# Kernel optimization log

Hardware: AMD Instinct MI355X
Metric: run time of the kernel (lower is better)

The kernel has to match this reference:

```python
import jax, jax.numpy as jnp
import numpy as np
import math

BATCH, SEQLEN, HID, STATE = 8, 4096, 1024, 64


def setup_inputs() -> dict:
    key = jax.random.key(0)
    k_u, k_a, k_b, k_c = jax.random.split(key, 4)
    u = jax.random.normal(k_u, (BATCH, SEQLEN, HID), dtype=jnp.float32)
    A = jax.random.normal(k_a, (HID, STATE), dtype=jnp.float32)
    Bm = jax.random.normal(k_b, (HID, STATE), dtype=jnp.float32)
    C = jax.random.normal(k_c, (HID, STATE), dtype=jnp.float32)
    Dv = jnp.zeros((HID,), dtype=jnp.float32)
    # buffer: dt = exp(linspace(log 1e-3, log 1e-1, state_size))
    dt = jnp.exp(jnp.linspace(math.log(0.001), math.log(0.1), STATE)).astype(jnp.float32)
    return {"u": u, "A": A, "Bm": Bm, "C": C, "Dv": Dv, "dt": dt}


def reference(u, A, Bm, C, Dv, dt):
    # Diagonal LTI SSM (ZOH discretization):
    #   A_cont = -exp(A)                         (Dh, N)
    #   dA = exp(A_cont * dt)                    (Dh, N)
    #   dB = Bm * (1 - dA) / (-A_cont)           (Dh, N)
    # recurrence: x_t = x_{t-1} * dA + u_t * dB;  y_t = sum_n C * x_t + Dv * u_t
    Aexp = jnp.exp(A)                 # -A_cont, positive
    dA = jnp.exp(-Aexp * dt[None, :])
    dB = Bm * (1.0 - dA) / Aexp

    B_, L, Dh = u.shape
    N = dA.shape[1]

    def step(x, u_t):
        # x: (B, Dh, N), u_t: (B, Dh)
        x = x * dA + u_t[..., None] * dB
        y = jnp.einsum('bdn,dn->bd', x, C)
        return x, y

    x0 = jnp.zeros((B_, Dh, N), dtype=u.dtype)
    _, ys = jax.lax.scan(step, x0, jnp.swapaxes(u, 0, 1))  # ys: (L, B, Dh)
    out = jnp.swapaxes(ys, 0, 1) + u * Dv[None, None, :]
    return out
```

## Files before the change

kernel.cpp:

```cpp
#include <hip/hip_runtime.h>
#include <math.h>

#define BATCH  8
#define SEQLEN 4096
#define HID    1024
#define STATE  64
#define NC     16
#define TC     (SEQLEN / NC)
#define TT     32
#define NTILE  (TC / TT)
#define DBLK   64
#define NS     16
#define NP     8
#define RB     8

typedef float f32x2 __attribute__((ext_vector_type(2)));
typedef float f32x4 __attribute__((ext_vector_type(4)));
typedef short bf16x8 __attribute__((ext_vector_type(8)));
typedef unsigned int u32x4 __attribute__((ext_vector_type(4)));

#define WS_PA   0
#define WS_PW   (256 * 1024)
#define WS_PE   (512 * 1024)
#define WS_PL2  (768 * 1024)
#define WS_ZL   (1ull  * 1024 * 1024)
#define WS_ZT   (36ull * 1024 * 1024)
#define WS_W2F  (56ull * 1024 * 1024)
#define WS_KRF  (92ull * 1024 * 1024)
#define WS_NEED (148ull * 1024 * 1024)

__device__ __forceinline__ unsigned int f2bf(float x) {
    unsigned int u = __builtin_bit_cast(unsigned int, x);
    u = (u + 0x7FFFu + ((u >> 16) & 1u)) >> 16;
    return u & 0xFFFFu;
}

__device__ __forceinline__ void gload_lds16(const void* g, void* l) {
    __builtin_amdgcn_global_load_lds((const __attribute__((address_space(1))) void*)g,
                                     (__attribute__((address_space(3))) void*)l,
                                     16, 0, 0);
}

__device__ __forceinline__ float quad_reduce_add(float y) {
    int t = __builtin_amdgcn_mov_dpp(__builtin_bit_cast(int, y), 0xB1, 0xF, 0xF, true);
    y += __builtin_bit_cast(float, t);
    t = __builtin_amdgcn_mov_dpp(__builtin_bit_cast(int, y), 0x4E, 0xF, 0xF, true);
    y += __builtin_bit_cast(float, t);
    return y;
}

__global__ void k0_params(const float* __restrict__ A, const float* __restrict__ Bm,
                          const float* __restrict__ C, const float* __restrict__ dt,
                          float* __restrict__ pa, float* __restrict__ pw,
                          float* __restrict__ pE, float* __restrict__ pl2) {
    int i = blockIdx.x * 256 + threadIdx.x;
    if (i >= HID * STATE) return;
    int n = i & (STATE - 1);
    float aexp = expf(A[i]);
    float dtn  = dt[n];
    float a    = expf(-aexp * dtn);
    pa[i]  = a;
    pw[i]  = C[i] * (Bm[i] * (1.0f - a) / aexp);
    pE[i]  = expf(-aexp * dtn * (float)TC);
    pl2[i] = -aexp * dtn * 1.44269504088896340736f;
}

__global__ __launch_bounds__(256, 3) void k1_locals(const float* __restrict__ u,
                                                    const float* __restrict__ pa,
                                                    float* __restrict__ zl) {
    __shared__ float utile[2][TT * DBLK];
    int bid  = blockIdx.x;
    int dset = bid & 15;
    int b    = (bid >> 4) & 7;
    int c    = bid >> 7;
    int w    = threadIdx.x >> 6;
    int lane = threadIdx.x & 63;
    int dl   = lane >> 2, p = lane & 3;
    int d    = dset * DBLK + w * 16 + dl;

    f32x2 a2[NP], z2[NP];
    {
        const f32x2* pap = (const f32x2*)(pa + (size_t)d * STATE + p * NS);
        #pragma unroll
        for (int j = 0; j < NP; j++) a2[j] = pap[j];
    }
    #pragma unroll
    for (int j = 0; j < NP; j++) { z2[j].x = 0.f; z2[j].y = 0.f; }

    const char* ubase = (const char*)(u + ((size_t)b * SEQLEN + (size_t)c * TC) * HID
                                        + (size_t)dset * DBLK);

    #define ISSUE_TILE(t, buf)                                                        \
        {                                                                             \
            _Pragma("unroll")                                                         \
            for (int k = 0; k < 2; k++) {                                             \
                int off = w * 2048 + k * 1024 + lane * 16;                            \
                int row = off >> 8;                                                   \
                int col = off & 255;                                                  \
                const float* src = (const float*)(ubase + ((size_t)((t) * TT + row)) * (HID * 4) + col); \
                float* dst = &utile[buf][w * 512 + k * 256];                           \
                gload_lds16(src, dst);                                                \
            }                                                                         \
        }

    ISSUE_TILE(0, 0);
    __syncthreads();
    int cur = 0;
    for (int tile = 0; tile < NTILE; ++tile) {
        if (tile + 1 < NTILE) ISSUE_TILE(tile + 1, cur ^ 1);
        const float* ut = &utile[cur][w * 16 + dl];
        #pragma unroll
        for (int r = 0; r < TT; r++) {
            float uss = ut[r * DBLK];
            f32x2 us; us.x = uss; us.y = uss;
            #pragma unroll
            for (int j = 0; j < NP; j++)
                z2[j] = __builtin_elementwise_fma(a2[j], z2[j], us);
        }
        __syncthreads();
        cur ^= 1;
    }

    f32x2* zp = (f32x2*)(zl + (((size_t)c * BATCH + b) * HID + d) * STATE + p * NS);
    #pragma unroll
    for (int j = 0; j < NP; j++) zp[j] = z2[j];
}

__global__ void k2_scan(const float* __restrict__ pE, float* __restrict__ zl) {
    int i  = blockIdx.x * 256 + threadIdx.x;
    int dn = i & (HID * STATE - 1);
    float E = pE[dn];
    size_t stride = (size_t)BATCH * HID * STATE;
    float g = zl[i];
    for (int c = 1; c < NC - 1; c++) {
        float v = zl[i + c * stride];
        g = fmaf(E, g, v);
        zl[i + c * stride] = g;
    }
}

__global__ void k2_zt(const float* __restrict__ pE, const float* __restrict__ zl,
                      unsigned short* __restrict__ ZT) {
    int i = blockIdx.x * 256 + threadIdx.x;
    int n = i & 63;
    int d = (i >> 6) & 1023;
    int b = i >> 16;
    float E = pE[d * 64 + n];
    size_t stride = (size_t)BATCH * HID * STATE;
    unsigned short* zt = ZT + (size_t)d * 8192 + (size_t)b * 1024 + n;
    zt[0] = 0;
    float g = zl[i];
    zt[64] = (unsigned short)f2bf(g);
    for (int c = 2; c < 16; c++) {
        g = fmaf(E, g, zl[i + (size_t)(c - 1) * stride]);
        zt[(size_t)c * 64] = (unsigned short)f2bf(g);
    }
}

__global__ void k_krf(const float* __restrict__ pw, const float* __restrict__ pl2,
                      const float* __restrict__ Dv, unsigned short* __restrict__ KRF) {
    __shared__ float wv[64], e2[64], K[256];
    int d = blockIdx.x, t = threadIdx.x;
    if (t < 64) { wv[t] = pw[d * 64 + t]; e2[t] = pl2[d * 64 + t]; }
    __syncthreads();
    float s = 0.0f;
    for (int n = 0; n < 64; n++) s += wv[n] * exp2f((float)t * e2[n]);
    if (t == 0) s += Dv[d];
    K[t] = s;
    __syncthreads();
    for (int idx = t; idx < 8192; idx += 256) {
        int j  = idx & 7;
        int ll = (idx >> 3) & 63;
        int m  = idx >> 9;
        int x  = (ll & 15) - 8 * (ll >> 4) + 16 * m - j;
        unsigned short v = 0;
        if (x >= 0) v = (unsigned short)f2bf(K[x]);
        KRF[(size_t)d * 8192 + idx] = v;
    }
}

__global__ void k_w2f(const float* __restrict__ pw, const float* __restrict__ pl2,
                      unsigned short* __restrict__ W2F) {
    __shared__ float wv[64], e2[64];
    int d = blockIdx.x, t = threadIdx.x;
    if (t < 64) { wv[t] = pw[d * 64 + t]; e2[t] = pl2[d * 64 + t]; }
    __syncthreads();
    for (int idx = t; idx < 16384; idx += 256) {
        int j  = idx & 7;
        int ll = (idx >> 3) & 63;
        int ns = (idx >> 9) & 1;
        int tt = idx >> 10;
        int n  = ns * 32 + 8 * (ll >> 4) + j;
        int tg = tt * 16 + (ll & 15);
        float val = wv[n] * exp2f((float)(tg + 1) * e2[n]);
        W2F[(size_t)d * 16384 + idx] = (unsigned short)f2bf(val);
    }
}

__global__ __launch_bounds__(1024, 1) void k3_mfma(const float* __restrict__ u,
                                                   const unsigned short* __restrict__ KRF,
                                                   const unsigned short* __restrict__ W2F,
                                                   const unsigned short* __restrict__ ZT,
                                                   float* __restrict__ out) {
    __shared__ __align__(16) char smem[131072];
    int bid = blockIdx.x;
    int dg  = bid & 63;
    int bcg = bid >> 6;
    int tid = threadIdx.x;
    int w   = tid >> 6;
    int l   = tid & 63;
    int g   = l >> 4, r16 = l & 15;
    int d   = dg * 16 + w;

    {
        int dl = tid & 15;
        int v  = (tid >> 4) & 63;
        int bc = v & 15;
        int sq = v >> 4;
        int gbc = bcg * 16 + bc;
        int bs = gbc >> 4, cs = gbc & 15;
        const float* up = u + ((size_t)(bs * SEQLEN + cs * TC + sq * 64)) * HID
                            + dg * 16 + dl;
        unsigned int rowb = (unsigned int)(dl * 16 + bc) * 512;
        #pragma unroll
        for (int kk = 0; kk < 8; kk++) {
            float uv[8];
            #pragma unroll
            for (int j = 0; j < 8; j++) uv[j] = up[(size_t)(kk * 8 + j) * HID];
            unsigned int pk[4];
            #pragma unroll
            for (int q = 0; q < 4; q++)
                pk[q] = f2bf(uv[2 * q]) | (f2bf(uv[2 * q + 1]) << 16);
            int sc   = sq * 8 + kk;
            int slot = (sc + 4 * (bc & 7) + 5 * dl) & 31;
            *(u32x4*)(&smem[rowb + slot * 16]) = (u32x4){pk[0], pk[1], pk[2], pk[3]};
        }
    }
    __syncthreads();

    f32x4 acc[16];
    #pragma unroll
    for (int tt = 0; tt < 16; tt++) acc[tt] = (f32x4){0.f, 0.f, 0.f, 0.f};

    const unsigned short* krf = KRF + (size_t)d * 8192 + l * 8;
    unsigned int rowr = (unsigned int)(w * 16 + r16) * 512;
    int rot = (4 * (r16 & 7) + 5 * w) & 31;

    {
        bf16x8 Af[8];
        #pragma unroll
        for (int mm = 0; mm < 8; mm++)
            Af[mm] = *(const bf16x8*)(krf + (size_t)mm * 512);
        #pragma unroll
        for (int mm = 0; mm < 8; mm++) {
            #pragma unroll
            for (int sk = 0; sk < 8; sk++) {
                if (2 * sk + mm <= 15) {
                    int slot = ((sk * 4 + g) + rot) & 31;
                    bf16x8 B = *(const bf16x8*)(&smem[rowr + slot * 16]);
                    acc[2 * sk + mm] =
                        __builtin_amdgcn_mfma_f32_16x16x32_bf16(Af[mm], B, acc[2 * sk + mm], 0, 0, 0);
                }
            }
        }
    }
    __builtin_amdgcn_sched_barrier(0);
    {
        bf16x8 Af[8];
        #pragma unroll
        for (int mm = 0; mm < 8; mm++)
            Af[mm] = *(const bf16x8*)(krf + (size_t)(8 + mm) * 512);
        #pragma unroll
        for (int mm = 0; mm < 8; mm++) {
            #pragma unroll
            for (int sk = 0; sk < 4; sk++) {
                if (2 * sk + 8 + mm <= 15) {
                    int slot = ((sk * 4 + g) + rot) & 31;
                    bf16x8 B = *(const bf16x8*)(&smem[rowr + slot * 16]);
                    acc[2 * sk + 8 + mm] =
                        __builtin_amdgcn_mfma_f32_16x16x32_bf16(Af[mm], B, acc[2 * sk + 8 + mm], 0, 0, 0);
                }
            }
        }
    }
    __builtin_amdgcn_sched_barrier(0);

    {
        const unsigned short* ztd = ZT + (size_t)d * 8192 + (size_t)bcg * 1024;
        bf16x8 Bz0 = *(const bf16x8*)(ztd + (size_t)r16 * 64 + 0 * 32 + 8 * g);
        bf16x8 Bz1 = *(const bf16x8*)(ztd + (size_t)r16 * 64 + 1 * 32 + 8 * g);
        const unsigned short* w2f = W2F + (size_t)d * 16384 + l * 8;
        #pragma unroll
        for (int grp = 0; grp < 4; grp++) {
            bf16x8 Aw[8];
            #pragma unroll
            for (int q = 0; q < 8; q++) {
                int tt = grp * 4 + (q >> 1);
                int ns = q & 1;
                Aw[q] = *(const bf16x8*)(w2f + (size_t)(tt * 2 + ns) * 512);
            }
            #pragma unroll
            for (int q = 0; q < 8; q++) {
                int tt = grp * 4 + (q >> 1);
                acc[grp * 4 + (q >> 1)] =
                    __builtin_amdgcn_mfma_f32_16x16x32_bf16(Aw[q], (q & 1) ? Bz1 : Bz0,
                                                            acc[tt], 0, 0, 0);
            }
            __builtin_amdgcn_sched_barrier(0);
        }
    }

    float* eps = (float*)smem;
    int p = tid >> 2, sub = tid & 3;
    int t16r = p >> 4, bcr = p & 15;
    int gbcr = bcg * 16 + bcr;
    int bo = gbcr >> 4, co = gbcr & 15;
    float* pout = out + ((size_t)(bo * SEQLEN + co * TC + t16r)) * HID + dg * 16 + sub * 4;
    #pragma unroll
    for (int tt = 0; tt < 16; tt++) {
        __syncthreads();
        #pragma unroll
        for (int rr = 0; rr < 4; rr++)
            eps[((g * 4 + rr) * 16 + r16) * 21 + w] = acc[tt][rr];
        __syncthreads();
        f32x4 vv;
        #pragma unroll
        for (int j = 0; j < 4; j++) vv[j] = eps[p * 21 + sub * 4 + j];
        *(f32x4*)(pout + (size_t)(tt * 16) * HID) = vv;
    }
}

__global__ __launch_bounds__(256, 3) void k3_scalar(const float* __restrict__ u,
                                                    const float* __restrict__ Dv,
                                                    const float* __restrict__ pa,
                                                    const float* __restrict__ pw,
                                                    const float* __restrict__ zl,
                                                    float* __restrict__ out) {
    __shared__ float utile[2][TT * DBLK];
    int bid  = blockIdx.x;
    int dset = bid & 15;
    int b    = (bid >> 4) & 7;
    int c    = bid >> 7;
    int w    = threadIdx.x >> 6;
    int lane = threadIdx.x & 63;
    int dl   = lane >> 2, p = lane & 3;
    int d    = dset * DBLK + w * 16 + dl;

    f32x2 a2[NP], w2[NP], z2[NP];
    {
        const f32x2* pap = (const f32x2*)(pa + (size_t)d * STATE + p * NS);
        const f32x2* pwp = (const f32x2*)(pw + (size_t)d * STATE + p * NS);
        #pragma unroll
        for (int j = 0; j < NP; j++) { a2[j] = pap[j]; w2[j] = pwp[j]; }
    }
    if (c == 0) {
        #pragma unroll
        for (int j = 0; j < NP; j++) { z2[j].x = 0.f; z2[j].y = 0.f; }
    } else {
        size_t stride = (size_t)BATCH * HID * STATE;
        const f32x2* zp = (const f32x2*)(zl + (size_t)(c - 1) * stride +
                                         ((size_t)b * HID + d) * STATE + p * NS);
        #pragma unroll
        for (int j = 0; j < NP; j++) z2[j] = zp[j];
    }

    float dvd = Dv[d];
    const char* ubase = (const char*)(u + ((size_t)b * SEQLEN + (size_t)c * TC) * HID
                                        + (size_t)dset * DBLK);
    float* po = out + ((size_t)b * SEQLEN + (size_t)c * TC) * HID + d;

    ISSUE_TILE(0, 0);
    __syncthreads();
    int cur = 0;
    for (int tile = 0; tile < NTILE; ++tile) {
        if (tile + 1 < NTILE) ISSUE_TILE(tile + 1, cur ^ 1);
        const float* ut = &utile[cur][w * 16 + dl];
        float* po_t = po + (size_t)tile * TT * HID;
        #pragma unroll
        for (int r0 = 0; r0 < TT; r0 += RB) {
            float ylane[RB], usv[RB];
            #pragma unroll
            for (int i = 0; i < RB; i++) {
                float uss = ut[(r0 + i) * DBLK];
                usv[i] = uss;
                f32x2 us; us.x = uss; us.y = uss;
                #pragma unroll
                for (int j = 0; j < NP; j++)
                    z2[j] = __builtin_elementwise_fma(a2[j], z2[j], us);
                f32x2 acc0 = z2[0] * w2[0];
                f32x2 acc1 = z2[1] * w2[1];
                #pragma unroll
                for (int j = 2; j < NP; j += 2) {
                    acc0 = __builtin_elementwise_fma(z2[j + 0], w2[j + 0], acc0);
                    acc1 = __builtin_elementwise_fma(z2[j + 1], w2[j + 1], acc1);
                }
                acc0 += acc1;
                ylane[i] = acc0.x + acc0.y;
            }
            #pragma unroll
            for (int i = 0; i < RB; i++) ylane[i] = quad_reduce_add(ylane[i]);
            #pragma unroll
            for (int i = 0; i < RB; i++)
                po_t[(size_t)(r0 + i) * HID] = fmaf(dvd, usv[i], ylane[i]);
        }
        __syncthreads();
        cur ^= 1;
    }
}

extern "C" void kernel_launch(void* const* d_in, const int* in_sizes, int n_in,
                              void* d_out, int out_size, void* d_ws, size_t ws_size,
                              hipStream_t stream) {
    const float* u  = (const float*)d_in[0];
    const float* A  = (const float*)d_in[1];
    const float* Bm = (const float*)d_in[2];
    const float* C  = (const float*)d_in[3];
    const float* Dv = (const float*)d_in[4];
    const float* dt = (const float*)d_in[5];
    float* out = (float*)d_out;

    char* ws = (char*)d_ws;
    float* pa  = (float*)(ws + WS_PA);
    float* pw  = (float*)(ws + WS_PW);
    float* pE  = (float*)(ws + WS_PE);
    float* pl2 = (float*)(ws + WS_PL2);
    float* zl  = (float*)(ws + WS_ZL);
    unsigned short* ZT  = (unsigned short*)(ws + WS_ZT);
    unsigned short* W2F = (unsigned short*)(ws + WS_W2F);
    unsigned short* KRF = (unsigned short*)(ws + WS_KRF);

    bool mfma = (ws_size >= WS_NEED);

    k0_params<<<(HID * STATE) / 256, 256, 0, stream>>>(A, Bm, C, dt, pa, pw, pE, pl2);
    k1_locals<<<16 * 8 * (NC - 1), 256, 0, stream>>>(u, pa, zl);

    if (mfma) {
        k_krf<<<1024, 256, 0, stream>>>(pw, pl2, Dv, KRF);
        k_w2f<<<1024, 256, 0, stream>>>(pw, pl2, W2F);
        k2_zt<<<(BATCH * HID * STATE) / 256, 256, 0, stream>>>(pE, zl, ZT);
        k3_mfma<<<512, 1024, 0, stream>>>(u, KRF, W2F, ZT, out);
    } else {
        k2_scan<<<(BATCH * HID * STATE) / 256, 256, 0, stream>>>(pE, zl);
        k3_scalar<<<16 * 8 * NC, 256, 0, stream>>>(u, Dv, pa, pw, zl, out);
    }
}
```

Measured before the change: 180.2 us.

## Halve k3_mfma block to 8 hidden channels, vectorize u loads, remap block order

The MFMA output kernel now uses 512-thread blocks covering 8 hidden channels instead of 16, with 64KB shared memory, and launches twice as many blocks. This lets more blocks be resident per CU. The u tile is staged with float4 loads instead of scalar strided loads, and the LDS swizzle and epilogue padding are re-derived for the new shape. Block indices are permuted so neighbouring blocks touch interleaved channel groups, which may change L2 or channel locality. The risk is worse output coalescing, since each row now writes only 32 bytes per block, and more redundant loads of ZT and KRF.

New measurement: 235.1 us. +30.5%, slower.

```diff
diff --git a/kernel.cpp b/kernel.cpp
--- a/kernel.cpp
+++ b/kernel.cpp
@@ -197,43 +197,49 @@
     }
 }
 
-__global__ __launch_bounds__(1024, 1) void k3_mfma(const float* __restrict__ u,
-                                                   const unsigned short* __restrict__ KRF,
-                                                   const unsigned short* __restrict__ W2F,
-                                                   const unsigned short* __restrict__ ZT,
-                                                   float* __restrict__ out) {
-    __shared__ __align__(16) char smem[131072];
+__global__ __launch_bounds__(512, 4) void k3_mfma(const float* __restrict__ u,
+                                                  const unsigned short* __restrict__ KRF,
+                                                  const unsigned short* __restrict__ W2F,
+                                                  const unsigned short* __restrict__ ZT,
+                                                  float* __restrict__ out) {
+    __shared__ __align__(16) char smem[65536];
     int bid = blockIdx.x;
-    int dg  = bid & 63;
-    int bcg = bid >> 6;
+    int qx  = bid & 7;
+    int r   = bid >> 3;
+    int p   = r & 15;
+    int bcg = r >> 4;
+    int dg  = (((p & 7) * 8 + qx) << 1) | (p >> 3);
     int tid = threadIdx.x;
     int w   = tid >> 6;
     int l   = tid & 63;
     int g   = l >> 4, r16 = l & 15;
-    int d   = dg * 16 + w;
-
-    {
-        int dl = tid & 15;
-        int v  = (tid >> 4) & 63;
-        int bc = v & 15;
-        int sq = v >> 4;
+    int d   = dg * 8 + w;
+
+    {
+        int dq = tid & 1;
+        int bc = (tid >> 1) & 15;
+        int sg = tid >> 5;
         int gbc = bcg * 16 + bc;
         int bs = gbc >> 4, cs = gbc & 15;
-        const float* up = u + ((size_t)(bs * SEQLEN + cs * TC + sq * 64)) * HID
-                            + dg * 16 + dl;
-        unsigned int rowb = (unsigned int)(dl * 16 + bc) * 512;
-        #pragma unroll
-        for (int kk = 0; kk < 8; kk++) {
-            float uv[8];
-            #pragma unroll
-            for (int j = 0; j < 8; j++) uv[j] = up[(size_t)(kk * 8 + j) * HID];
-            unsigned int pk[4];
-            #pragma unroll
-            for (int q = 0; q < 4; q++)
-                pk[q] = f2bf(uv[2 * q]) | (f2bf(uv[2 * q + 1]) << 16);
-            int sc   = sq * 8 + kk;
-            int slot = (sc + 4 * (bc & 7) + 5 * dl) & 31;
-            *(u32x4*)(&smem[rowb + slot * 16]) = (u32x4){pk[0], pk[1], pk[2], pk[3]};
+        const f32x4* up = (const f32x4*)(u + ((size_t)(bs * SEQLEN + cs * TC + sg * 16)) * HID
+                                           + dg * 8 + dq * 4);
+        #pragma unroll
+        for (int half = 0; half < 2; half++) {
+            f32x4 v[8];
+            #pragma unroll
+            for (int j = 0; j < 8; j++) v[j] = up[(size_t)(half * 8 + j) * 256];
+            #pragma unroll
+            for (int dd = 0; dd < 4; dd++) {
+                unsigned int pk[4];
+                #pragma unroll
+                for (int q = 0; q < 4; q++)
+                    pk[q] = f2bf(v[2 * q][dd]) | (f2bf(v[2 * q + 1][dd]) << 16);
+                int dloc = dq * 4 + dd;
+                int sc   = sg * 2 + half;
+                int slot = (sc + 5 * bc + 3 * dloc) & 31;
+                *(u32x4*)(&smem[(unsigned)((dloc * 16 + bc) * 512) + slot * 16]) =
+                    (u32x4){pk[0], pk[1], pk[2], pk[3]};
+            }
         }
     }
     __syncthreads();
@@ -243,8 +249,8 @@
     for (int tt = 0; tt < 16; tt++) acc[tt] = (f32x4){0.f, 0.f, 0.f, 0.f};
 
     const unsigned short* krf = KRF + (size_t)d * 8192 + l * 8;
-    unsigned int rowr = (unsigned int)(w * 16 + r16) * 512;
-    int rot = (4 * (r16 & 7) + 5 * w) & 31;
+    unsigned int rowr = (unsigned)(w * 16 + r16) * 512;
+    int rot = (5 * r16 + 3 * w) & 31;
 
     {
         bf16x8 Af[8];
@@ -302,30 +308,30 @@
             #pragma unroll
             for (int q = 0; q < 8; q++) {
                 int tt = grp * 4 + (q >> 1);
-                acc[grp * 4 + (q >> 1)] =
-                    __builtin_amdgcn_mfma_f32_16x16x32_bf16(Aw[q], (q & 1) ? Bz1 : Bz0,
-                                                            acc[tt], 0, 0, 0);
+                acc[tt] = __builtin_amdgcn_mfma_f32_16x16x32_bf16(Aw[q], (q & 1) ? Bz1 : Bz0,
+                                                                  acc[tt], 0, 0, 0);
             }
             __builtin_amdgcn_sched_barrier(0);
         }
     }
 
     float* eps = (float*)smem;
-    int p = tid >> 2, sub = tid & 3;
-    int t16r = p >> 4, bcr = p & 15;
-    int gbcr = bcg * 16 + bcr;
+    int dhalf = tid & 1;
+    int bcr   = (tid >> 1) & 15;
+    int t16r  = tid >> 5;
+    int gbcr  = bcg * 16 + bcr;
     int bo = gbcr >> 4, co = gbcr & 15;
-    float* pout = out + ((size_t)(bo * SEQLEN + co * TC + t16r)) * HID + dg * 16 + sub * 4;
+    float* pout = out + ((size_t)(bo * SEQLEN + co * TC + t16r)) * HID + dg * 8 + dhalf * 4;
     #pragma unroll
     for (int tt = 0; tt < 16; tt++) {
         __syncthreads();
         #pragma unroll
         for (int rr = 0; rr < 4; rr++)
-            eps[((g * 4 + rr) * 16 + r16) * 21 + w] = acc[tt][rr];
+            eps[(4 * g + rr) * 147 + r16 * 9 + w] = acc[tt][rr];
         __syncthreads();
         f32x4 vv;
         #pragma unroll
-        for (int j = 0; j < 4; j++) vv[j] = eps[p * 21 + sub * 4 + j];
+        for (int j = 0; j < 4; j++) vv[j] = eps[t16r * 147 + bcr * 9 + dhalf * 4 + j];
         *(f32x4*)(pout + (size_t)(tt * 16) * HID) = vv;
     }
 }
@@ -438,7 +444,7 @@
         k_krf<<<1024, 256, 0, stream>>>(pw, pl2, Dv, KRF);
         k_w2f<<<1024, 256, 0, stream>>>(pw, pl2, W2F);
         k2_zt<<<(BATCH * HID * STATE) / 256, 256, 0, stream>>>(pE, zl, ZT);
-        k3_mfma<<<512, 1024, 0, stream>>>(u, KRF, W2F, ZT, out);
+        k3_mfma<<<1024, 512, 0, stream>>>(u, KRF, W2F, ZT, out);
     } else {
         k2_scan<<<(BATCH * HID * STATE) / 256, 256, 0, stream>>>(pE, zl);
         k3_scalar<<<16 * 8 * NC, 256, 0, stream>>>(u, Dv, pa, pw, zl, out);
```

## Emit bf16 pre-swizzled u from chunk-state kernel and stream it via LDS DMA

Applied to the files above, without the earlier changes.

The chunk-state kernel now runs over all 16 chunks. While it has each u tile in LDS, it also converts the tile to bf16 and writes it to a workspace buffer in the layout the MFMA kernel expects. The MFMA kernel then loads that buffer straight into shared memory with global_load_lds, instead of doing strided fp32 gathers and converting them itself, and its swizzle rotation is changed to match. This drops one full fp32 read of u and the conversion work from k3, at the cost of an extra bf16 write and read, one more chunk of k1 work, and an added barrier per tile in k1.

New measurement: 162.2 us. 1.11x faster.

```diff
diff --git a/kernel.cpp b/kernel.cpp
--- a/kernel.cpp
+++ b/kernel.cpp
@@ -24,10 +24,11 @@
 #define WS_PE   (512 * 1024)
 #define WS_PL2  (768 * 1024)
 #define WS_ZL   (1ull  * 1024 * 1024)
-#define WS_ZT   (36ull * 1024 * 1024)
-#define WS_W2F  (56ull * 1024 * 1024)
-#define WS_KRF  (92ull * 1024 * 1024)
-#define WS_NEED (148ull * 1024 * 1024)
+#define WS_KRF  (1ull  * 1024 * 1024)
+#define WS_W2F  (31ull * 1024 * 1024)
+#define WS_ZT   (63ull * 1024 * 1024)
+#define WS_UBF  (79ull * 1024 * 1024)
+#define WS_NEED (143ull * 1024 * 1024)
 
 __device__ __forceinline__ unsigned int f2bf(float x) {
     unsigned int u = __builtin_bit_cast(unsigned int, x);
@@ -67,8 +68,10 @@
 
 __global__ __launch_bounds__(256, 3) void k1_locals(const float* __restrict__ u,
                                                     const float* __restrict__ pa,
-                                                    float* __restrict__ zl) {
+                                                    float* __restrict__ zl,
+                                                    unsigned short* __restrict__ ubf) {
     __shared__ float utile[2][TT * DBLK];
+    __shared__ unsigned int lds_pk[64 * 17];
     int bid  = blockIdx.x;
     int dset = bid & 15;
     int b    = (bid >> 4) & 7;
@@ -117,13 +120,34 @@
             for (int j = 0; j < NP; j++)
                 z2[j] = __builtin_elementwise_fma(a2[j], z2[j], us);
         }
+        if (ubf != nullptr) {
+            int cw   = w * 16 + (lane & 15);
+            int tgrp = lane >> 4;
+            const float* colp = &utile[cur][cw];
+            #pragma unroll
+            for (int q = 0; q < 4; q++) {
+                int r0 = tgrp * 8 + 2 * q;
+                unsigned int pk = f2bf(colp[r0 * DBLK]) | (f2bf(colp[(r0 + 1) * DBLK]) << 16);
+                lds_pk[cw * 17 + tgrp * 4 + q] = pk;
+            }
+            __syncthreads();
+            int dcol = threadIdx.x >> 2, jj = threadIdx.x & 3;
+            u32x4 vv;
+            #pragma unroll
+            for (int k = 0; k < 4; k++) vv[k] = lds_pk[dcol * 17 + jj * 4 + k];
+            unsigned short* dst = ubf + ((((size_t)(b * 16 + c) * 8 + tile) * 1024
+                                          + dset * 64) * 32);
+            *(u32x4*)((char*)dst + threadIdx.x * 16) = vv;
+        }
         __syncthreads();
         cur ^= 1;
     }
 
-    f32x2* zp = (f32x2*)(zl + (((size_t)c * BATCH + b) * HID + d) * STATE + p * NS);
-    #pragma unroll
-    for (int j = 0; j < NP; j++) zp[j] = z2[j];
+    if (c < NC - 1) {
+        f32x2* zp = (f32x2*)(zl + (((size_t)c * BATCH + b) * HID + d) * STATE + p * NS);
+        #pragma unroll
+        for (int j = 0; j < NP; j++) zp[j] = z2[j];
+    }
 }
 
 __global__ void k2_scan(const float* __restrict__ pE, float* __restrict__ zl) {
@@ -197,7 +221,7 @@
     }
 }
 
-__global__ __launch_bounds__(1024, 1) void k3_mfma(const float* __restrict__ u,
+__global__ __launch_bounds__(1024, 1) void k3_mfma(const unsigned short* __restrict__ ubf,
                                                    const unsigned short* __restrict__ KRF,
                                                    const unsigned short* __restrict__ W2F,
                                                    const unsigned short* __restrict__ ZT,
@@ -213,27 +237,17 @@
     int d   = dg * 16 + w;
 
     {
-        int dl = tid & 15;
-        int v  = (tid >> 4) & 63;
-        int bc = v & 15;
-        int sq = v >> 4;
-        int gbc = bcg * 16 + bc;
-        int bs = gbc >> 4, cs = gbc & 15;
-        const float* up = u + ((size_t)(bs * SEQLEN + cs * TC + sq * 64)) * HID
-                            + dg * 16 + dl;
-        unsigned int rowb = (unsigned int)(dl * 16 + bc) * 512;
-        #pragma unroll
-        for (int kk = 0; kk < 8; kk++) {
-            float uv[8];
-            #pragma unroll
-            for (int j = 0; j < 8; j++) uv[j] = up[(size_t)(kk * 8 + j) * HID];
-            unsigned int pk[4];
-            #pragma unroll
-            for (int q = 0; q < 4; q++)
-                pk[q] = f2bf(uv[2 * q]) | (f2bf(uv[2 * q + 1]) << 16);
-            int sc   = sq * 8 + kk;
-            int slot = (sc + 4 * (bc & 7) + 5 * dl) & 31;
-            *(u32x4*)(&smem[rowb + slot * 16]) = (u32x4){pk[0], pk[1], pk[2], pk[3]};
+        int h = l >> 5, q = l & 31;
+        #pragma unroll
+        for (int i = 0; i < 8; i++) {
+            int bc = 2 * i + h;
+            int sc = (q - 5 * bc - 3 * w) & 31;
+            int gbc = bcg * 16 + bc;
+            const char* src = (const char*)ubf
+                + (((size_t)(gbc * 8 + (sc >> 2)) * 1024) + dg * 16 + w) * 64
+                + (sc & 3) * 16;
+            char* dst = &smem[(unsigned)(w * 16 + 2 * i) * 512];
+            gload_lds16(src, dst);
         }
     }
     __syncthreads();
@@ -244,7 +258,7 @@
 
     const unsigned short* krf = KRF + (size_t)d * 8192 + l * 8;
     unsigned int rowr = (unsigned int)(w * 16 + r16) * 512;
-    int rot = (4 * (r16 & 7) + 5 * w) & 31;
+    int rot = (5 * r16 + 3 * w) & 31;
 
     {
         bf16x8 Af[8];
@@ -302,9 +316,8 @@
             #pragma unroll
             for (int q = 0; q < 8; q++) {
                 int tt = grp * 4 + (q >> 1);
-                acc[grp * 4 + (q >> 1)] =
-                    __builtin_amdgcn_mfma_f32_16x16x32_bf16(Aw[q], (q & 1) ? Bz1 : Bz0,
-                                                            acc[tt], 0, 0, 0);
+                acc[tt] = __builtin_amdgcn_mfma_f32_16x16x32_bf16(Aw[q], (q & 1) ? Bz1 : Bz0,
+                                                                  acc[tt], 0, 0, 0);
             }
             __builtin_amdgcn_sched_barrier(0);
         }
@@ -425,21 +438,23 @@
     float* pE  = (float*)(ws + WS_PE);
     float* pl2 = (float*)(ws + WS_PL2);
     float* zl  = (float*)(ws + WS_ZL);
+    unsigned short* KRF = (unsigned short*)(ws + WS_KRF);
+    unsigned short* W2F = (unsigned short*)(ws + WS_W2F);
     unsigned short* ZT  = (unsigned short*)(ws + WS_ZT);
-    unsigned short* W2F = (unsigned short*)(ws + WS_W2F);
-    unsigned short* KRF = (unsigned short*)(ws + WS_KRF);
+    unsigned short* UBF = (unsigned short*)(ws + WS_UBF);
 
     bool mfma = (ws_size >= WS_NEED);
 
     k0_params<<<(HID * STATE) / 256, 256, 0, stream>>>(A, Bm, C, dt, pa, pw, pE, pl2);
-    k1_locals<<<16 * 8 * (NC - 1), 256, 0, stream>>>(u, pa, zl);
 
     if (mfma) {
+        k1_locals<<<16 * 8 * NC, 256, 0, stream>>>(u, pa, zl, UBF);
+        k2_zt<<<(BATCH * HID * STATE) / 256, 256, 0, stream>>>(pE, zl, ZT);
         k_krf<<<1024, 256, 0, stream>>>(pw, pl2, Dv, KRF);
         k_w2f<<<1024, 256, 0, stream>>>(pw, pl2, W2F);
-        k2_zt<<<(BATCH * HID * STATE) / 256, 256, 0, stream>>>(pE, zl, ZT);
-        k3_mfma<<<512, 1024, 0, stream>>>(u, KRF, W2F, ZT, out);
+        k3_mfma<<<512, 1024, 0, stream>>>(UBF, KRF, W2F, ZT, out);
     } else {
+        k1_locals<<<16 * 8 * (NC - 1), 256, 0, stream>>>(u, pa, zl, nullptr);
         k2_scan<<<(BATCH * HID * STATE) / 256, 256, 0, stream>>>(pE, zl);
         k3_scalar<<<16 * 8 * NC, 256, 0, stream>>>(u, Dv, pa, pw, zl, out);
     }
```
